# Kernel optimization log

Hardware: AMD Instinct MI355X
Metric: run time of the kernel (lower is better)

The kernel has to match this reference:

```python
import math
import jax, jax.numpy as jnp
import numpy as np

BS, N, D, H = 4, 512, 1024, 16
HD = D // H


def setup_inputs() -> dict:
    key = jax.random.key(0)
    ks = jax.random.split(key, 12)
    s = 1.0 / math.sqrt(D)
    return {
        "x": jax.random.normal(ks[0], (BS, N, D), jnp.float32),
        "r": jax.random.normal(ks[1], (BS, 3, N, N), jnp.float32),
        "bias": jax.random.normal(ks[2], (BS, H, N, N), jnp.float32),
        "mask": jax.random.randint(ks[3], (BS, 1, N, N), 0, 2, jnp.int32),
        "wq": jax.random.normal(ks[4], (D, D), jnp.float32) * s,
        "bq": jnp.zeros((D,), jnp.float32),
        "wk": jax.random.normal(ks[5], (D, D), jnp.float32) * s,
        "bk": jnp.zeros((D,), jnp.float32),
        "wv": jax.random.normal(ks[6], (D, D), jnp.float32) * s,
        "bv": jnp.zeros((D,), jnp.float32),
        "wo": jax.random.normal(ks[7], (D, 1), jnp.float32) * s,
        "bo": jnp.zeros((1,), jnp.float32),
    }


def reference(x, r, bias, mask, wq, bq, wk, bk, wv, bv, wo, bo):
    bs, n, d = x.shape
    # projections -> (bs, h, n, hd)
    q = (x @ wq + bq).reshape(bs, n, H, HD).transpose(0, 2, 1, 3)
    k = (x @ wk + bk).reshape(bs, n, H, HD).transpose(0, 2, 1, 3)
    v = (x @ wv + bv).reshape(bs, n, H, HD).transpose(0, 2, 1, 3)
    logits = jnp.einsum("bhid,bhjd->bhij", q, k) / math.sqrt(HD) + bias
    logits = jnp.where(mask == 0, jnp.float32(-1e9), logits)
    w = jax.nn.softmax(logits, axis=-1)  # (bs,h,n,n)
    # o[b,i,c,h,d] = sum_j r[b,c,i,j] * w[b,h,i,j] * v[b,h,j,d]
    o = jnp.einsum("bcij,bhij,bhjd->bichd", r, w, v)
    o = o.reshape(bs, n, 3, d)
    force = o @ wo + bo  # (bs, n, 3, 1)
    return force
```

## Files before the change

kernel.cpp:

```cpp
#include <hip/hip_runtime.h>
#include <stdint.h>

#define BSZ 4
#define NSEQ 512
#define DMOD 1024
#define NH 16
#define HD 64

typedef __attribute__((ext_vector_type(8))) short bf16x8;
typedef __attribute__((ext_vector_type(4))) float f32x4;

__device__ __forceinline__ unsigned short f2bf(float f) {
    union { float f; uint32_t u; } v; v.f = f;
    uint32_t u = v.u;
    u += 0x7FFFu + ((u >> 16) & 1u);
    return (unsigned short)(u >> 16);
}

__device__ __forceinline__ void gload_lds16(const unsigned short* g, unsigned short* l) {
    __builtin_amdgcn_global_load_lds(
        (const __attribute__((address_space(1))) void*)g,
        (__attribute__((address_space(3))) void*)l, 16, 0, 0);
}

__device__ __forceinline__ void gload_lds16f(const float* g, float* l) {
    __builtin_amdgcn_global_load_lds(
        (const __attribute__((address_space(1))) void*)g,
        (__attribute__((address_space(3))) void*)l, 16, 0, 0);
}

#define LGKM_BAR() do { \
    asm volatile("s_waitcnt lgkmcnt(0)" ::: "memory"); \
    __builtin_amdgcn_sched_barrier(0); \
    __builtin_amdgcn_s_barrier(); \
    __builtin_amdgcn_sched_barrier(0); } while (0)

__global__ __launch_bounds__(256) void k_prep(
        const float* __restrict__ x, const float* __restrict__ wq, const float* __restrict__ wk,
        const float* __restrict__ wv, const float* __restrict__ bv, const float* __restrict__ wo,
        unsigned short* __restrict__ xb, unsigned short* __restrict__ wqt,
        unsigned short* __restrict__ wkt, float* __restrict__ wv2t, float* __restrict__ bv2) {
    __shared__ float t[32][33];
    int bx = blockIdx.x, tid = threadIdx.x;
    if (bx < 2048) {
        int i = bx * 256 + tid;
        float4 v = ((const float4*)x)[i];
        ushort4 o; o.x = f2bf(v.x); o.y = f2bf(v.y); o.z = f2bf(v.z); o.w = f2bf(v.w);
        ((ushort4*)xb)[i] = o;
    } else if (bx < 4096) {
        int g = bx - 2048; int z = g >> 10; g &= 1023;
        const float* src = z ? wk : wq;
        unsigned short* dst = z ? wkt : wqt;
        int be = (g & 31) * 32, bc = (g >> 5) * 32;
        int tx = tid & 31, ty = tid >> 5;
        #pragma unroll
        for (int yy = 0; yy < 32; yy += 8)
            t[ty + yy][tx] = src[(size_t)(be + ty + yy) * DMOD + bc + tx];
        __syncthreads();
        #pragma unroll
        for (int yy = 0; yy < 32; yy += 8)
            dst[(size_t)(bc + ty + yy) * DMOD + be + tx] = f2bf(t[tx][ty + yy]);
    } else {
        int g = bx - 4096;
        int grp = tid >> 6, l = tid & 63;
        int e = g * 4 + grp;
        float out = 0.f;
        #pragma unroll
        for (int it = 0; it < 16; ++it) {
            float v = wv[(size_t)e * DMOD + it * 64 + l] * wo[it * 64 + l];
            #pragma unroll
            for (int off = 1; off < 64; off <<= 1) v += __shfl_xor(v, off, 64);
            if (l == it) out = v;
        }
        if (l < 16) wv2t[l * DMOD + e] = out;
        if (g == 0 && grp == 0) {
            float ob = 0.f;
            #pragma unroll
            for (int it = 0; it < 16; ++it) {
                float v = bv[it * 64 + l] * wo[it * 64 + l];
                #pragma unroll
                for (int off = 1; off < 64; off <<= 1) v += __shfl_xor(v, off, 64);
                if (l == it) ob = v;
            }
            if (l < 16) bv2[l] = ob;
        }
    }
}

__global__ __launch_bounds__(256, 3) void k_mid(
        const float* __restrict__ x, const float* __restrict__ wv2t, const float* __restrict__ bv2,
        const unsigned short* __restrict__ xb, const unsigned short* __restrict__ wqt,
        const unsigned short* __restrict__ wkt, const float* __restrict__ bq,
        const float* __restrict__ bk, float* __restrict__ u,
        unsigned short* __restrict__ qT, unsigned short* __restrict__ kT) {
    __shared__ unsigned short lA[128 * 64];
    __shared__ unsigned short lB[128 * 64];
    int bx = blockIdx.x, tid = threadIdx.x;
    if (bx >= 256) {
        int wave = (bx - 256) * 4 + (tid >> 6);
        int l = tid & 63;
        int b = wave >> 9, j = wave & 511;
        const float* xr = x + (size_t)(b * NSEQ + j) * DMOD;
        float p[16];
        #pragma unroll
        for (int h = 0; h < 16; ++h) p[h] = 0.f;
        for (int it = 0; it < 16; ++it) {
            int e = l + it * 64;
            float xv = xr[e];
            #pragma unroll
            for (int h = 0; h < 16; ++h) p[h] += xv * wv2t[h * DMOD + e];
        }
        #pragma unroll
        for (int h = 0; h < 16; ++h) {
            #pragma unroll
            for (int off = 1; off < 64; off <<= 1) p[h] += __shfl_xor(p[h], off, 64);
        }
        float out = 0.f;
        #pragma unroll
        for (int h = 0; h < 16; ++h) if (l == h) out = p[h] + bv2[h];
        if (l < 16) u[(b * 16 + l) * NSEQ + j] = out;
        return;
    }
    int g = bx;
    int mt = g & 15, nt8 = (g >> 4) & 7, z = g >> 7;
    const unsigned short* Wt = z ? wkt : wqt;
    const float* bias = z ? bk : bq;
    unsigned short* outT = z ? kT : qT;
    float scale = z ? 1.f : 0.125f;
    int m0 = mt * 128, n0 = nt8 * 128;
    int w = tid >> 6, lane = tid & 63;
    int wr = w >> 1, wc = w & 1;
    int quad = lane >> 4, cs = lane & 15;
    int l8 = lane >> 3, l7 = lane & 7;
    int sg = l7 ^ l8;

    f32x4 acc[4][4];
    #pragma unroll
    for (int mi = 0; mi < 4; ++mi)
        #pragma unroll
        for (int ni = 0; ni < 4; ++ni) acc[mi][ni] = (f32x4){0.f, 0.f, 0.f, 0.f};

    for (int kc = 0; kc < 16; ++kc) {
        int k0 = kc * 64;
        #pragma unroll
        for (int q = 0; q < 4; ++q) {
            int row = w * 32 + q * 8 + l8;
            gload_lds16(xb + (size_t)(m0 + row) * DMOD + k0 + sg * 8,
                        &lA[(w * 32 + q * 8) * 64]);
            gload_lds16(Wt + (size_t)(n0 + row) * DMOD + k0 + sg * 8,
                        &lB[(w * 32 + q * 8) * 64]);
        }
        __syncthreads();
        #pragma unroll
        for (int ks = 0; ks < 2; ++ks) {
            bf16x8 af[4], bfr[4];
            #pragma unroll
            for (int mi = 0; mi < 4; ++mi) {
                int row = wr * 64 + mi * 16 + cs;
                int gq = (ks * 4 + quad) ^ (row & 7);
                af[mi] = *(const bf16x8*)&lA[row * 64 + gq * 8];
            }
            #pragma unroll
            for (int ni = 0; ni < 4; ++ni) {
                int row = wc * 64 + ni * 16 + cs;
                int gq = (ks * 4 + quad) ^ (row & 7);
                bfr[ni] = *(const bf16x8*)&lB[row * 64 + gq * 8];
            }
            #pragma unroll
            for (int mi = 0; mi < 4; ++mi)
                #pragma unroll
                for (int ni = 0; ni < 4; ++ni)
                    acc[mi][ni] = __builtin_amdgcn_mfma_f32_16x16x32_bf16(
                        af[mi], bfr[ni], acc[mi][ni], 0, 0, 0);
        }
        __syncthreads();
    }
    #pragma unroll
    for (int ni = 0; ni < 4; ++ni) {
        int n = n0 + wc * 64 + ni * 16 + cs;
        int h = n >> 6, d = n & 63;
        float bvv = bias[n];
        #pragma unroll
        for (int mi = 0; mi < 4; ++mi) {
            #pragma unroll
            for (int rr = 0; rr < 4; ++rr) {
                int mg = m0 + wr * 64 + mi * 16 + quad * 4 + rr;
                int b = mg >> 9, i = mg & 511;
                outT[(size_t)((b * 16 + h) * NSEQ + i) * HD + d] =
                    f2bf((acc[mi][ni][rr] + bvv) * scale);
            }
        }
    }
}

#define BGRP 264
#define BHEAD 1056
__global__ __launch_bounds__(512, 4) void k_attn(
        const unsigned short* __restrict__ qT, const unsigned short* __restrict__ kT,
        const float* __restrict__ bias, const int* __restrict__ mask,
        const float* __restrict__ u, const float* __restrict__ r,
        float* __restrict__ spart, float* __restrict__ P) {
    __shared__ float bias_lds[8 * BHEAD];
    __shared__ float rT4[16 * 64 * 4];
    int tid = threadIdx.x;
    int w = tid >> 6, lane = tid & 63;
    int quad = lane >> 4, col = lane & 15;
    int it = blockIdx.x, jc = blockIdx.y, bz = blockIdx.z;
    int b = bz >> 1, hg = bz & 1;
    int i0 = it * 16, j0 = jc * 64;
    int h = hg * 8 + w;
    int bh = b * 16 + h;

    float s0[2], s1[2], s2[2], smf[2];
    const float* rbase = r + (size_t)b * 3 * NSEQ * NSEQ;
    const int* mrow = mask + (size_t)b * NSEQ * NSEQ;
    #pragma unroll
    for (int t = 0; t < 2; ++t) {
        int slot = t * 512 + tid;
        int il = slot >> 6, jl = slot & 63;
        size_t off = (size_t)(i0 + il) * NSEQ + j0 + jl;
        s0[t] = rbase[off];
        s1[t] = rbase[(size_t)NSEQ * NSEQ + off];
        s2[t] = rbase[2 * (size_t)NSEQ * NSEQ + off];
        smf[t] = (float)mrow[off];
    }

    const unsigned short* qbase = qT + ((size_t)(bh * NSEQ + i0 + col)) * HD + quad * 8;
    bf16x8 a0 = *(const bf16x8*)qbase;
    bf16x8 a1 = *(const bf16x8*)(qbase + 32);
    bf16x8 kf0[4], kf1[4];
    #pragma unroll
    for (int jt = 0; jt < 4; ++jt) {
        const unsigned short* kbase =
            kT + ((size_t)(bh * NSEQ + j0 + jt * 16 + col)) * HD + quad * 8;
        kf0[jt] = *(const bf16x8*)kbase;
        kf1[jt] = *(const bf16x8*)(kbase + 32);
    }
    const float* ub = u + (size_t)bh * NSEQ;
    float uvv[4];
    #pragma unroll
    for (int jt = 0; jt < 4; ++jt) uvv[jt] = ub[j0 + jt * 16 + col];

    {
        const float* bsrc = bias + (size_t)bh * NSEQ * NSEQ;
        int il4 = lane >> 4, jl4 = (lane & 15) * 4;
        #pragma unroll
        for (int g = 0; g < 4; ++g)
            gload_lds16f(bsrc + (size_t)(i0 + g * 4 + il4) * NSEQ + j0 + jl4,
                         &bias_lds[w * BHEAD + g * BGRP]);
    }

    #pragma unroll
    for (int t = 0; t < 2; ++t) {
        int slot = t * 512 + tid;
        float4 pk; pk.x = s0[t]; pk.y = s1[t]; pk.z = s2[t]; pk.w = smf[t];
        *(float4*)&rT4[slot * 4] = pk;
    }

    LGKM_BAR();
    asm volatile("s_waitcnt vmcnt(0)" ::: "memory");
    __builtin_amdgcn_sched_barrier(0);

    const float* bwave = &bias_lds[w * BHEAD];
    float sp[4] = {0.f, 0.f, 0.f, 0.f};
    float pc0[4] = {0.f, 0.f, 0.f, 0.f};
    float pc1[4] = {0.f, 0.f, 0.f, 0.f};
    float pc2[4] = {0.f, 0.f, 0.f, 0.f};
    #pragma unroll
    for (int jt = 0; jt < 4; ++jt) {
        f32x4 acc = (f32x4){0.f, 0.f, 0.f, 0.f};
        acc = __builtin_amdgcn_mfma_f32_16x16x32_bf16(a0, kf0[jt], acc, 0, 0, 0);
        acc = __builtin_amdgcn_mfma_f32_16x16x32_bf16(a1, kf1[jt], acc, 0, 0, 0);
        float uv = uvv[jt];
        int jl = jt * 16 + col;
        #pragma unroll
        for (int rr = 0; rr < 4; ++rr) {
            int il = quad * 4 + rr;
            float4 v = *(const float4*)&rT4[(il * 64 + jl) * 4];
            float bvv = bwave[quad * BGRP + rr * 64 + jl];
            float lg = acc[rr] + bvv;
            float e = __expf(lg) * v.w;
            sp[rr] += e;
            float eu = e * uv;
            pc0[rr] += eu * v.x;
            pc1[rr] += eu * v.y;
            pc2[rr] += eu * v.z;
        }
    }
    #pragma unroll
    for (int rr = 0; rr < 4; ++rr) {
        #pragma unroll
        for (int off = 1; off < 16; off <<= 1) {
            sp[rr]  += __shfl_xor(sp[rr], off, 64);
            pc0[rr] += __shfl_xor(pc0[rr], off, 64);
            pc1[rr] += __shfl_xor(pc1[rr], off, 64);
            pc2[rr] += __shfl_xor(pc2[rr], off, 64);
        }
    }
    if (col == 0) {
        #pragma unroll
        for (int rr = 0; rr < 4; ++rr) {
            int il = quad * 4 + rr;
            spart[((size_t)bh * NSEQ + i0 + il) * 8 + jc] = sp[rr];
            size_t pb = ((((size_t)bh * 32 + it) * 16 + il) * 8 + jc) * 3;
            P[pb + 0] = pc0[rr];
            P[pb + 1] = pc1[rr];
            P[pb + 2] = pc2[rr];
        }
    }
}

__global__ __launch_bounds__(256) void k_final(
        const float* __restrict__ spart, const float* __restrict__ P,
        const float* __restrict__ bo, float* __restrict__ out) {
    __shared__ float part[4][16][3];
    int bx = blockIdx.x;
    int b = bx >> 5, it = bx & 31;
    int tid = threadIdx.x;
    int il = tid & 15, h = tid >> 4;
    int w = tid >> 6;
    int bh = b * 16 + h;
    int i = it * 16 + il;
    const float* sprow = spart + ((size_t)bh * NSEQ + i) * 8;
    float4 sa = *(const float4*)sprow;
    float4 sb = *(const float4*)(sprow + 4);
    float s = sa.x + sa.y + sa.z + sa.w + sb.x + sb.y + sb.z + sb.w;
    float sinv = (s > 0.f) ? 1.f / s : 0.f;
    const float* pbase = P + (((size_t)bh * 32 + it) * 16 + il) * 24;
    float f[3] = {0.f, 0.f, 0.f};
    #pragma unroll
    for (int q = 0; q < 6; ++q) {
        float4 v = *(const float4*)(pbase + q * 4);
        f[(q * 4 + 0) % 3] += v.x;
        f[(q * 4 + 1) % 3] += v.y;
        f[(q * 4 + 2) % 3] += v.z;
        f[(q * 4 + 3) % 3] += v.w;
    }
    f[0] *= sinv; f[1] *= sinv; f[2] *= sinv;
    #pragma unroll
    for (int c = 0; c < 3; ++c) {
        f[c] += __shfl_xor(f[c], 16, 64);
        f[c] += __shfl_xor(f[c], 32, 64);
    }
    if ((tid & 48) == 0) {
        part[w][il][0] = f[0]; part[w][il][1] = f[1]; part[w][il][2] = f[2];
    }
    __syncthreads();
    if (tid < 16) {
        float bov = bo[0];
        float o0 = part[0][tid][0] + part[1][tid][0] + part[2][tid][0] + part[3][tid][0];
        float o1 = part[0][tid][1] + part[1][tid][1] + part[2][tid][1] + part[3][tid][1];
        float o2 = part[0][tid][2] + part[1][tid][2] + part[2][tid][2] + part[3][tid][2];
        size_t row = (size_t)b * NSEQ + it * 16 + tid;
        out[row * 3 + 0] = o0 + bov;
        out[row * 3 + 1] = o1 + bov;
        out[row * 3 + 2] = o2 + bov;
    }
}

extern "C" void kernel_launch(void* const* d_in, const int* in_sizes, int n_in,
                              void* d_out, int out_size, void* d_ws, size_t ws_size,
                              hipStream_t stream) {
    const float* x    = (const float*)d_in[0];
    const float* rr   = (const float*)d_in[1];
    const float* bias = (const float*)d_in[2];
    const int*   mask = (const int*)d_in[3];
    const float* wq   = (const float*)d_in[4];
    const float* bq   = (const float*)d_in[5];
    const float* wk   = (const float*)d_in[6];
    const float* bk   = (const float*)d_in[7];
    const float* wv   = (const float*)d_in[8];
    const float* bv   = (const float*)d_in[9];
    const float* wo   = (const float*)d_in[10];
    const float* bo   = (const float*)d_in[11];
    float* out = (float*)d_out;

    char* ws = (char*)d_ws;
    unsigned short* xb    = (unsigned short*)(ws + 0);
    unsigned short* wqt   = (unsigned short*)(ws + 4194304);
    unsigned short* wkt   = (unsigned short*)(ws + 6291456);
    float*          wv2t  = (float*)(ws + 8388608);
    float*          bv2   = (float*)(ws + 8454144);
    float*          u     = (float*)(ws + 8454400);
    unsigned short* qT    = (unsigned short*)(ws + 8585472);
    unsigned short* kT    = (unsigned short*)(ws + 12779776);
    float*          spart = (float*)(ws + 16974080);
    float*          P     = (float*)(ws + 18022656);

    k_prep<<<4352, 256, 0, stream>>>(x, wq, wk, wv, bv, wo, xb, wqt, wkt, wv2t, bv2);
    k_mid<<<768, 256, 0, stream>>>(x, wv2t, bv2, xb, wqt, wkt, bq, bk, u, qT, kT);
    k_attn<<<dim3(32, 8, 8), 512, 0, stream>>>(qT, kT, bias, mask, u, rr, spart, P);
    k_final<<<128, 256, 0, stream>>>(spart, P, bo, out);
}
```

Before: 186.7 us.

## Pre-pack r and mask into per-tile float4 buffer in prep kernel

Adds a k_prep stage that packs the three r channels and the mask into a tiled float4 layout in workspace. k_attn then reads each lane's packed values directly into registers instead of staging them through LDS with a block barrier. This is meant to remove the LDS transpose and barrier and to cut redundant r/mask loads across the two head groups. The cost is an extra write and read of a 16 MB buffer, and the launch-bounds occupancy hint on k_attn is dropped.

```diff
diff --git a/kernel.cpp b/kernel.cpp
--- a/kernel.cpp
+++ b/kernel.cpp
@@ -29,17 +29,13 @@
         (__attribute__((address_space(3))) void*)l, 16, 0, 0);
 }
 
-#define LGKM_BAR() do { \
-    asm volatile("s_waitcnt lgkmcnt(0)" ::: "memory"); \
-    __builtin_amdgcn_sched_barrier(0); \
-    __builtin_amdgcn_s_barrier(); \
-    __builtin_amdgcn_sched_barrier(0); } while (0)
-
 __global__ __launch_bounds__(256) void k_prep(
         const float* __restrict__ x, const float* __restrict__ wq, const float* __restrict__ wk,
         const float* __restrict__ wv, const float* __restrict__ bv, const float* __restrict__ wo,
+        const float* __restrict__ r, const int* __restrict__ mask,
         unsigned short* __restrict__ xb, unsigned short* __restrict__ wqt,
-        unsigned short* __restrict__ wkt, float* __restrict__ wv2t, float* __restrict__ bv2) {
+        unsigned short* __restrict__ wkt, float* __restrict__ wv2t, float* __restrict__ bv2,
+        float4* __restrict__ rpk) {
     __shared__ float t[32][33];
     int bx = blockIdx.x, tid = threadIdx.x;
     if (bx < 2048) {
@@ -60,7 +56,7 @@
         #pragma unroll
         for (int yy = 0; yy < 32; yy += 8)
             dst[(size_t)(bc + ty + yy) * DMOD + be + tx] = f2bf(t[tx][ty + yy]);
-    } else {
+    } else if (bx < 4352) {
         int g = bx - 4096;
         int grp = tid >> 6, l = tid & 63;
         int e = g * 4 + grp;
@@ -83,6 +79,24 @@
                 if (l == it) ob = v;
             }
             if (l < 16) bv2[l] = ob;
+        }
+    } else {
+        int g = bx - 4352;
+        int b = g >> 8, it = (g >> 3) & 31, jc = g & 7;
+        const float* rb = r + (size_t)b * 3 * NSEQ * NSEQ;
+        const int* mrow = mask + (size_t)b * NSEQ * NSEQ;
+        float4* dst = rpk + ((size_t)g << 10);
+        #pragma unroll
+        for (int tq = 0; tq < 4; ++tq) {
+            int slot = tq * 256 + tid;
+            int il = slot >> 6, jl = slot & 63;
+            size_t off = (size_t)(it * 16 + il) * NSEQ + jc * 64 + jl;
+            float4 pk;
+            pk.x = rb[off];
+            pk.y = rb[(size_t)NSEQ * NSEQ + off];
+            pk.z = rb[2 * (size_t)NSEQ * NSEQ + off];
+            pk.w = (float)mrow[off];
+            dst[slot] = pk;
         }
     }
 }
@@ -195,13 +209,12 @@
 
 #define BGRP 264
 #define BHEAD 1056
-__global__ __launch_bounds__(512, 4) void k_attn(
+__global__ __launch_bounds__(512) void k_attn(
         const unsigned short* __restrict__ qT, const unsigned short* __restrict__ kT,
-        const float* __restrict__ bias, const int* __restrict__ mask,
-        const float* __restrict__ u, const float* __restrict__ r,
+        const float* __restrict__ bias, const float4* __restrict__ rpk,
+        const float* __restrict__ u,
         float* __restrict__ spart, float* __restrict__ P) {
-    __shared__ float bias_lds[8 * BHEAD];
-    __shared__ float rT4[16 * 64 * 4];
+    __shared__ float blds[8 * BHEAD];
     int tid = threadIdx.x;
     int w = tid >> 6, lane = tid & 63;
     int quad = lane >> 4, col = lane & 15;
@@ -211,58 +224,44 @@
     int h = hg * 8 + w;
     int bh = b * 16 + h;
 
-    float s0[2], s1[2], s2[2], smf[2];
-    const float* rbase = r + (size_t)b * 3 * NSEQ * NSEQ;
-    const int* mrow = mask + (size_t)b * NSEQ * NSEQ;
-    #pragma unroll
-    for (int t = 0; t < 2; ++t) {
-        int slot = t * 512 + tid;
-        int il = slot >> 6, jl = slot & 63;
-        size_t off = (size_t)(i0 + il) * NSEQ + j0 + jl;
-        s0[t] = rbase[off];
-        s1[t] = rbase[(size_t)NSEQ * NSEQ + off];
-        s2[t] = rbase[2 * (size_t)NSEQ * NSEQ + off];
-        smf[t] = (float)mrow[off];
+    {
+        const float* bsrc = bias + ((size_t)bh * NSEQ + i0) * NSEQ + j0;
+        int il4 = lane >> 4, jl4 = (lane & 15) * 4;
+        #pragma unroll
+        for (int g4 = 0; g4 < 4; ++g4)
+            gload_lds16f(bsrc + (size_t)(g4 * 4 + il4) * NSEQ + jl4,
+                         &blds[w * BHEAD + g4 * BGRP]);
     }
 
     const unsigned short* qbase = qT + ((size_t)(bh * NSEQ + i0 + col)) * HD + quad * 8;
     bf16x8 a0 = *(const bf16x8*)qbase;
     bf16x8 a1 = *(const bf16x8*)(qbase + 32);
+    const unsigned short* kbh = kT + (size_t)bh * NSEQ * HD;
     bf16x8 kf0[4], kf1[4];
+    float uvv[4];
+    const float* ub = u + (size_t)bh * NSEQ;
     #pragma unroll
     for (int jt = 0; jt < 4; ++jt) {
-        const unsigned short* kbase =
-            kT + ((size_t)(bh * NSEQ + j0 + jt * 16 + col)) * HD + quad * 8;
-        kf0[jt] = *(const bf16x8*)kbase;
-        kf1[jt] = *(const bf16x8*)(kbase + 32);
-    }
-    const float* ub = u + (size_t)bh * NSEQ;
-    float uvv[4];
-    #pragma unroll
-    for (int jt = 0; jt < 4; ++jt) uvv[jt] = ub[j0 + jt * 16 + col];
-
-    {
-        const float* bsrc = bias + (size_t)bh * NSEQ * NSEQ;
-        int il4 = lane >> 4, jl4 = (lane & 15) * 4;
-        #pragma unroll
-        for (int g = 0; g < 4; ++g)
-            gload_lds16f(bsrc + (size_t)(i0 + g * 4 + il4) * NSEQ + j0 + jl4,
-                         &bias_lds[w * BHEAD + g * BGRP]);
-    }
-
-    #pragma unroll
-    for (int t = 0; t < 2; ++t) {
-        int slot = t * 512 + tid;
-        float4 pk; pk.x = s0[t]; pk.y = s1[t]; pk.z = s2[t]; pk.w = smf[t];
-        *(float4*)&rT4[slot * 4] = pk;
-    }
-
-    LGKM_BAR();
+        const unsigned short* kb = kbh + ((size_t)(j0 + jt * 16 + col)) * HD + quad * 8;
+        kf0[jt] = *(const bf16x8*)kb;
+        kf1[jt] = *(const bf16x8*)(kb + 32);
+        uvv[jt] = ub[j0 + jt * 16 + col];
+    }
+
+    int tg = (b << 8) + (it << 3) + jc;
+    const float4* rt = rpk + ((size_t)tg << 10);
+    float4 rpx[16];
+    #pragma unroll
+    for (int jt = 0; jt < 4; ++jt)
+        #pragma unroll
+        for (int rr = 0; rr < 4; ++rr)
+            rpx[jt * 4 + rr] = rt[(quad * 4 + rr) * 64 + jt * 16 + col];
+
     asm volatile("s_waitcnt vmcnt(0)" ::: "memory");
     __builtin_amdgcn_sched_barrier(0);
 
-    const float* bwave = &bias_lds[w * BHEAD];
-    float sp[4] = {0.f, 0.f, 0.f, 0.f};
+    const float* bwave = &blds[w * BHEAD];
+    float sp[4]  = {0.f, 0.f, 0.f, 0.f};
     float pc0[4] = {0.f, 0.f, 0.f, 0.f};
     float pc1[4] = {0.f, 0.f, 0.f, 0.f};
     float pc2[4] = {0.f, 0.f, 0.f, 0.f};
@@ -275,8 +274,7 @@
         int jl = jt * 16 + col;
         #pragma unroll
         for (int rr = 0; rr < 4; ++rr) {
-            int il = quad * 4 + rr;
-            float4 v = *(const float4*)&rT4[(il * 64 + jl) * 4];
+            float4 v = rpx[jt * 4 + rr];
             float bvv = bwave[quad * BGRP + rr * 64 + jl];
             float lg = acc[rr] + bvv;
             float e = __expf(lg) * v.w;
@@ -302,10 +300,10 @@
         for (int rr = 0; rr < 4; ++rr) {
             int il = quad * 4 + rr;
             spart[((size_t)bh * NSEQ + i0 + il) * 8 + jc] = sp[rr];
-            size_t pb = ((((size_t)bh * 32 + it) * 16 + il) * 8 + jc) * 3;
-            P[pb + 0] = pc0[rr];
-            P[pb + 1] = pc1[rr];
-            P[pb + 2] = pc2[rr];
+            size_t pb2 = ((((size_t)bh * 32 + it) * 16 + il) * 8 + jc) * 3;
+            P[pb2 + 0] = pc0[rr];
+            P[pb2 + 1] = pc1[rr];
+            P[pb2 + 2] = pc2[rr];
         }
     }
 }
@@ -386,9 +384,11 @@
     unsigned short* kT    = (unsigned short*)(ws + 12779776);
     float*          spart = (float*)(ws + 16974080);
     float*          P     = (float*)(ws + 18022656);
-
-    k_prep<<<4352, 256, 0, stream>>>(x, wq, wk, wv, bv, wo, xb, wqt, wkt, wv2t, bv2);
+    float4*         rpk   = (float4*)(ws + 21168384);
+
+    k_prep<<<5376, 256, 0, stream>>>(x, wq, wk, wv, bv, wo, rr, mask,
+                                     xb, wqt, wkt, wv2t, bv2, rpk);
     k_mid<<<768, 256, 0, stream>>>(x, wv2t, bv2, xb, wqt, wkt, bq, bk, u, qT, kT);
-    k_attn<<<dim3(32, 8, 8), 512, 0, stream>>>(qT, kT, bias, mask, u, rr, spart, P);
+    k_attn<<<dim3(32, 8, 8), 512, 0, stream>>>(qT, kT, bias, rpk, u, spart, P);
     k_final<<<128, 256, 0, stream>>>(spart, P, bo, out);
 }
```

Measured after the change: 195.4 us. 4.7% more time.
